# Kernel optimization log

Hardware: AMD Instinct MI355X
Metric: run time of the kernel (lower is better)

Reference implementation:

```python
import jax, jax.numpy as jnp
import numpy as np

# SqueezeSeg CRF config
NUM_CLASS = 4
SIZE_Z, SIZE_A = 3, 5            # LCN_HEIGHT, LCN_WIDTH
B, H, W = 16, 64, 512            # batch, zenith, azimuth
RCRF_ITER = 3
BI_FILTER_COEF = 0.1
ANG_FILTER_COEF = 0.02
ANG_THETA_A = 0.9
BILATERAL_THETA_A = 0.9
K = SIZE_Z * SIZE_A              # 15 -> 14 neighbors (center excluded)

# neighbor offsets of the 3x5 condensing kernel, center excluded
OFFSETS = [(dz, da) for dz in range(SIZE_Z) for da in range(SIZE_A)
           if not (dz == SIZE_Z // 2 and da == SIZE_A // 2)]

def _gauss_weights(theta_sq):
    # angular_filter_kernel: Gaussian of squared spatial offset, center zeroed
    g = [np.exp(-((dz - SIZE_Z // 2) ** 2 + (da - SIZE_A // 2) ** 2) / (2.0 * theta_sq))
         for dz, da in OFFSETS]
    return jnp.asarray(np.array(g, dtype=np.float32))

def gather_neighbors(x):
    # x: [B,C,H,W] -> [B,C,K-1,H,W]; zero-padded 'same' neighborhood gather
    pz, pa = SIZE_Z // 2, SIZE_A // 2
    xp = jnp.pad(x, ((0, 0), (0, 0), (pz, pz), (pa, pa)))
    return jnp.stack([xp[:, :, dz:dz + H, da:da + W] for dz, da in OFFSETS], axis=2)

def setup_inputs() -> dict:
    key = jax.random.key(0)
    k1, k2, k3 = jax.random.split(key, 3)
    x = jax.random.normal(k1, (B, NUM_CLASS, H, W), dtype=jnp.float32)
    bilateral_filters = jax.random.uniform(k2, (B, 1, K - 1, H, W), dtype=jnp.float32)
    lidar_mask = (jax.random.uniform(k3, (B, 1, H, W)) > 0.5).astype(jnp.float32)
    return {"x": x, "bilateral_filters": bilateral_filters, "lidar_mask": lidar_mask}

def reference(x, bilateral_filters, lidar_mask):
    g_ang = _gauss_weights(ANG_THETA_A ** 2)
    g_bi = _gauss_weights(BILATERAL_THETA_A ** 2)
    compat = jnp.ones((NUM_CLASS, NUM_CLASS), jnp.float32) - jnp.eye(NUM_CLASS, dtype=jnp.float32)
    ang_compat = compat * ANG_FILTER_COEF   # [out_class, in_class] 1x1 conv
    bi_compat = compat * BI_FILTER_COEF

    for _ in range(RCRF_ITER):
        unary = jax.nn.softmax(x, axis=1)                     # softmax over class dim
        nb = gather_neighbors(unary)                          # [B,C,14,H,W]
        # depthwise angular filters = Gaussian-weighted neighbor sums
        ang = jnp.einsum('k,bckhw->bchw', g_ang, nb)
        bi_ang = jnp.einsum('k,bckhw->bchw', g_bi, nb)
        # condensing conv on masked unary, weighted by per-pixel bilateral filters
        nb_m = gather_neighbors(unary * lidar_mask)           # [B,C,14,H,W]
        condensed = jnp.sum(nb_m * bilateral_filters, axis=2) # [B,C,H,W]
        bi = condensed * lidar_mask * bi_ang
        # 1x1 compatibility transforms
        ang2 = jnp.einsum('oc,bchw->bohw', ang_compat, ang)
        bi2 = jnp.einsum('oc,bchw->bohw', bi_compat, bi)
        x = unary + ang2 + bi2
    return x
```

## Files before the change

### kernel.cpp

```cpp
#include <hip/hip_runtime.h>


#define NCLASS 4
#define HH 64
#define WW 512
#define BB 16
#define TH 8
#define TW 64
#define UR (TH + 6)
#define UC (TW + 12)
#define PLANE (HH * WW)

#define G1 0.53940412f
#define G2 0.29095687f
#define G4 0.08466190f
#define G5 0.04566227f

__device__ __forceinline__ void fma4(float4& d, float s, const float4& v) {
    d.x = fmaf(s, v.x, d.x);
    d.y = fmaf(s, v.y, d.y);
    d.z = fmaf(s, v.z, d.z);
    d.w = fmaf(s, v.w, d.w);
}

template <bool SM>
__device__ __forceinline__ float4 crf_combine(const float4 A, const float4 C,
                                              const float4 u, const float mcen)
{
    const float bx = C.x * mcen * A.x;
    const float by = C.y * mcen * A.y;
    const float bz = C.z * mcen * A.z;
    const float bw = C.w * mcen * A.w;
    const float sa = A.x + A.y + A.z + A.w;
    const float sb = bx + by + bz + bw;
    float4 r;
    r.x = u.x + 0.02f * (sa - A.x) + 0.1f * (sb - bx);
    r.y = u.y + 0.02f * (sa - A.y) + 0.1f * (sb - by);
    r.z = u.z + 0.02f * (sa - A.z) + 0.1f * (sb - bz);
    r.w = u.w + 0.02f * (sa - A.w) + 0.1f * (sb - bw);
    if (SM) {
        const float mx  = fmaxf(fmaxf(r.x, r.y), fmaxf(r.z, r.w));
        const float e0  = __expf(r.x - mx);
        const float e1  = __expf(r.y - mx);
        const float e2  = __expf(r.z - mx);
        const float e3  = __expf(r.w - mx);
        const float inv = 1.0f / (e0 + e1 + e2 + e3);
        r = make_float4(e0 * inv, e1 * inv, e2 * inv, e3 * inv);
    }
    return r;
}

template <int MR, int MC, bool FINAL>
__device__ __forceinline__ void crf_step(
    float4 (*__restrict__ u_lds)[UC], const float (*__restrict__ m_lds)[UC],
    const float* __restrict__ filt, float* __restrict__ dst,
    int b, int h0, int w0, int tid)
{
    constexpr int RH  = TH + 2 * MR;
    constexpr int RW  = TW + 2 * MC;
    constexpr int GPR = RW / 2;
    constexpr int NG  = RH * GPR;
    constexpr int NS  = (NG + 255) / 256;

    const float GE[5] = {G5, G2, G1, G2, G5};
    const float GC[5] = {G4, G1, 0.f, G1, G4};

    float4 xa[NS], xb[NS];

#pragma unroll
    for (int j = 0; j < NS; ++j) {
        const int s = tid + 256 * j;
        float4 r0 = make_float4(0.f, 0.f, 0.f, 0.f);
        float4 r1 = make_float4(0.f, 0.f, 0.f, 0.f);
        int gh = -1, gw = -1;
        if (s < NG) {
            const int lr = s / GPR;
            const int gc = s - lr * GPR;
            const int lc = 2 * gc;
            gh = h0 + lr - MR;
            gw = w0 + lc - MC;
            const int ur = lr + (3 - MR);
            const int uc = lc + (6 - MC);
            if (gh >= 0 && gh < HH && gw >= 0 && gw < WW) {
                const float* fp = filt + ((size_t)b * 14 * HH + gh) * WW + gw;
                float2 f[14];
#pragma unroll
                for (int k = 0; k < 14; ++k)
                    f[k] = *reinterpret_cast<const float2*>(fp + (size_t)k * PLANE);

                float4 A0 = make_float4(0.f, 0.f, 0.f, 0.f);
                float4 A1 = A0, C0 = A0, C1 = A0;
                float4 ucen0 = A0, ucen1 = A0;
                float  mcen0 = 0.f, mcen1 = 0.f;

#pragma unroll
                for (int dz = -1; dz <= 1; ++dz) {
                    const int rr = ur + dz;
                    float4 U[6];
                    float  M[6];
#pragma unroll
                    for (int t = 0; t < 6; ++t) U[t] = u_lds[rr][uc - 2 + t];
#pragma unroll
                    for (int t = 0; t < 3; ++t) {
                        const float2 mm =
                            *reinterpret_cast<const float2*>(&m_lds[rr][uc - 2 + 2 * t]);
                        M[2 * t]     = mm.x;
                        M[2 * t + 1] = mm.y;
                    }
                    if (dz == 0) { ucen0 = U[2]; ucen1 = U[3]; mcen0 = M[2]; mcen1 = M[3]; }
#pragma unroll
                    for (int t = 0; t < 5; ++t) {
                        if (dz == 0 && t == 2) continue;
                        const int   k  = (dz == -1) ? t
                                       : (dz == 0)  ? 5 + (t > 2 ? t - 1 : t)
                                                    : 9 + t;
                        const float gk = (dz == 0) ? GC[t] : GE[t];
                        const float fm0 = f[k].x * M[t];
                        const float fm1 = f[k].y * M[t + 1];
                        fma4(A0, gk,  U[t]);      fma4(C0, fm0, U[t]);
                        fma4(A1, gk,  U[t + 1]);  fma4(C1, fm1, U[t + 1]);
                    }
                }
                r0 = crf_combine<!FINAL>(A0, C0, ucen0, mcen0);
                r1 = crf_combine<!FINAL>(A1, C1, ucen1, mcen1);

                if (FINAL) {
                    float* o = dst + ((size_t)b * NCLASS * HH + gh) * WW + gw;
                    *reinterpret_cast<float2*>(o)             = make_float2(r0.x, r1.x);
                    *reinterpret_cast<float2*>(o + PLANE)     = make_float2(r0.y, r1.y);
                    *reinterpret_cast<float2*>(o + 2 * PLANE) = make_float2(r0.z, r1.z);
                    *reinterpret_cast<float2*>(o + 3 * PLANE) = make_float2(r0.w, r1.w);
                }
            }
        }
        if (!FINAL) { xa[j] = r0; xb[j] = r1; }
    }

    if (!FINAL) {
        __syncthreads();
#pragma unroll
        for (int j = 0; j < NS; ++j) {
            const int s = tid + 256 * j;
            if (s < NG) {
                const int lr = s / GPR;
                const int gc = s - lr * GPR;
                const int lc = 2 * gc;
                u_lds[lr + (3 - MR)][lc + (6 - MC)]     = xa[j];
                u_lds[lr + (3 - MR)][lc + (6 - MC) + 1] = xb[j];
            }
        }
        __syncthreads();
    }
}

__global__ __launch_bounds__(256, 4) void crf_fused(
    const float* __restrict__ xin,
    const float* __restrict__ filt,
    const float* __restrict__ mask,
    float* __restrict__ xout)
{
    __shared__ float4 u_lds[UR][UC];
    __shared__ float  m_lds[UR][UC];

    const int b   = blockIdx.z;
    const int h0  = blockIdx.y * TH;
    const int w0  = blockIdx.x * TW;
    const int tid = threadIdx.x;

    constexpr int NP = (UR * UC) / 2;
    for (int idx = tid; idx < NP; idx += 256) {
        const int lr = idx / (UC / 2);
        const int lc = 2 * (idx - lr * (UC / 2));
        const int gh = h0 + lr - 3;
        const int gw = w0 + lc - 6;
        float4 u0 = make_float4(0.f, 0.f, 0.f, 0.f);
        float4 u1 = u0;
        float2 mm = make_float2(0.f, 0.f);
        if (gh >= 0 && gh < HH && gw >= 0 && gw < WW) {
            const float* px = xin + ((size_t)b * NCLASS * HH + gh) * WW + gw;
            const float2 v0 = *reinterpret_cast<const float2*>(px);
            const float2 v1 = *reinterpret_cast<const float2*>(px + PLANE);
            const float2 v2 = *reinterpret_cast<const float2*>(px + 2 * PLANE);
            const float2 v3 = *reinterpret_cast<const float2*>(px + 3 * PLANE);
            mm = *reinterpret_cast<const float2*>(mask + ((size_t)b * HH + gh) * WW + gw);
            {
                const float mx  = fmaxf(fmaxf(v0.x, v1.x), fmaxf(v2.x, v3.x));
                const float e0  = __expf(v0.x - mx);
                const float e1  = __expf(v1.x - mx);
                const float e2  = __expf(v2.x - mx);
                const float e3  = __expf(v3.x - mx);
                const float inv = 1.0f / (e0 + e1 + e2 + e3);
                u0 = make_float4(e0 * inv, e1 * inv, e2 * inv, e3 * inv);
            }
            {
                const float mx  = fmaxf(fmaxf(v0.y, v1.y), fmaxf(v2.y, v3.y));
                const float e0  = __expf(v0.y - mx);
                const float e1  = __expf(v1.y - mx);
                const float e2  = __expf(v2.y - mx);
                const float e3  = __expf(v3.y - mx);
                const float inv = 1.0f / (e0 + e1 + e2 + e3);
                u1 = make_float4(e0 * inv, e1 * inv, e2 * inv, e3 * inv);
            }
        }
        u_lds[lr][lc]     = u0;
        u_lds[lr][lc + 1] = u1;
        *reinterpret_cast<float2*>(&m_lds[lr][lc]) = mm;
    }
    __syncthreads();

    crf_step<2, 4, false>(u_lds, m_lds, filt, xout, b, h0, w0, tid);
    crf_step<1, 2, false>(u_lds, m_lds, filt, xout, b, h0, w0, tid);
    crf_step<0, 0, true >(u_lds, m_lds, filt, xout, b, h0, w0, tid);
}

extern "C" void kernel_launch(void* const* d_in, const int* in_sizes, int n_in,
                              void* d_out, int out_size, void* d_ws, size_t ws_size,
                              hipStream_t stream) {
    const float* x    = (const float*)d_in[0];
    const float* filt = (const float*)d_in[1];
    const float* msk  = (const float*)d_in[2];
    float* out = (float*)d_out;
    (void)d_ws; (void)ws_size;

    dim3 grid(WW / TW, HH / TH, BB);
    dim3 block(256);
    crf_fused<<<grid, block, 0, stream>>>(x, filt, msk, out);
}
```

Before: 100.0 us.

## Map one thread per pixel pair and load bilateral filters once for all CRF iterations

Switches to 512-thread blocks with a fixed pixel-pair assignment per thread covering the largest halo region (12x72). Each thread loads its 14 bilateral filter values into registers once and reuses them across all three CRF iterations, instead of reloading them from global memory every iteration. Later iterations, which cover smaller regions, leave some threads idle, and holding the filters in registers raises register pressure at 512 threads per block.

Measured after the change: 96.14 us. -3.9%, faster.

```diff
diff --git a/kernel.cpp b/kernel.cpp
--- a/kernel.cpp
+++ b/kernel.cpp
@@ -10,6 +10,10 @@
 #define UR (TH + 6)
 #define UC (TW + 12)
 #define PLANE (HH * WW)
+#define R1H 12
+#define R1W 72
+#define GPR1 (R1W / 2)
+#define NPAIR1 (R1H * GPR1)
 
 #define G1 0.53940412f
 #define G2 0.29095687f
@@ -53,107 +57,83 @@
 template <int MR, int MC, bool FINAL>
 __device__ __forceinline__ void crf_step(
     float4 (*__restrict__ u_lds)[UC], const float (*__restrict__ m_lds)[UC],
-    const float* __restrict__ filt, float* __restrict__ dst,
-    int b, int h0, int w0, int tid)
+    const float2* __restrict__ f, float* __restrict__ dst,
+    int b, int lr1, int lc1, int gh, int gw, bool inb)
 {
-    constexpr int RH  = TH + 2 * MR;
-    constexpr int RW  = TW + 2 * MC;
-    constexpr int GPR = RW / 2;
-    constexpr int NG  = RH * GPR;
-    constexpr int NS  = (NG + 255) / 256;
+    constexpr int RH = TH + 2 * MR;
+    constexpr int RW = TW + 2 * MC;
+    constexpr int LR_LO = 2 - MR, LR_HI = 2 - MR + RH;
+    constexpr int LC_LO = 4 - MC, LC_HI = 4 - MC + RW;
+
+    const bool act = inb && lr1 >= LR_LO && lr1 < LR_HI
+                         && lc1 >= LC_LO && (lc1 + 1) < LC_HI;
 
     const float GE[5] = {G5, G2, G1, G2, G5};
     const float GC[5] = {G4, G1, 0.f, G1, G4};
 
-    float4 xa[NS], xb[NS];
-
-#pragma unroll
-    for (int j = 0; j < NS; ++j) {
-        const int s = tid + 256 * j;
-        float4 r0 = make_float4(0.f, 0.f, 0.f, 0.f);
-        float4 r1 = make_float4(0.f, 0.f, 0.f, 0.f);
-        int gh = -1, gw = -1;
-        if (s < NG) {
-            const int lr = s / GPR;
-            const int gc = s - lr * GPR;
-            const int lc = 2 * gc;
-            gh = h0 + lr - MR;
-            gw = w0 + lc - MC;
-            const int ur = lr + (3 - MR);
-            const int uc = lc + (6 - MC);
-            if (gh >= 0 && gh < HH && gw >= 0 && gw < WW) {
-                const float* fp = filt + ((size_t)b * 14 * HH + gh) * WW + gw;
-                float2 f[14];
-#pragma unroll
-                for (int k = 0; k < 14; ++k)
-                    f[k] = *reinterpret_cast<const float2*>(fp + (size_t)k * PLANE);
-
-                float4 A0 = make_float4(0.f, 0.f, 0.f, 0.f);
-                float4 A1 = A0, C0 = A0, C1 = A0;
-                float4 ucen0 = A0, ucen1 = A0;
-                float  mcen0 = 0.f, mcen1 = 0.f;
-
-#pragma unroll
-                for (int dz = -1; dz <= 1; ++dz) {
-                    const int rr = ur + dz;
-                    float4 U[6];
-                    float  M[6];
-#pragma unroll
-                    for (int t = 0; t < 6; ++t) U[t] = u_lds[rr][uc - 2 + t];
-#pragma unroll
-                    for (int t = 0; t < 3; ++t) {
-                        const float2 mm =
-                            *reinterpret_cast<const float2*>(&m_lds[rr][uc - 2 + 2 * t]);
-                        M[2 * t]     = mm.x;
-                        M[2 * t + 1] = mm.y;
-                    }
-                    if (dz == 0) { ucen0 = U[2]; ucen1 = U[3]; mcen0 = M[2]; mcen1 = M[3]; }
-#pragma unroll
-                    for (int t = 0; t < 5; ++t) {
-                        if (dz == 0 && t == 2) continue;
-                        const int   k  = (dz == -1) ? t
-                                       : (dz == 0)  ? 5 + (t > 2 ? t - 1 : t)
-                                                    : 9 + t;
-                        const float gk = (dz == 0) ? GC[t] : GE[t];
-                        const float fm0 = f[k].x * M[t];
-                        const float fm1 = f[k].y * M[t + 1];
-                        fma4(A0, gk,  U[t]);      fma4(C0, fm0, U[t]);
-                        fma4(A1, gk,  U[t + 1]);  fma4(C1, fm1, U[t + 1]);
-                    }
-                }
-                r0 = crf_combine<!FINAL>(A0, C0, ucen0, mcen0);
-                r1 = crf_combine<!FINAL>(A1, C1, ucen1, mcen1);
-
-                if (FINAL) {
-                    float* o = dst + ((size_t)b * NCLASS * HH + gh) * WW + gw;
-                    *reinterpret_cast<float2*>(o)             = make_float2(r0.x, r1.x);
-                    *reinterpret_cast<float2*>(o + PLANE)     = make_float2(r0.y, r1.y);
-                    *reinterpret_cast<float2*>(o + 2 * PLANE) = make_float2(r0.z, r1.z);
-                    *reinterpret_cast<float2*>(o + 3 * PLANE) = make_float2(r0.w, r1.w);
-                }
-            }
-        }
-        if (!FINAL) { xa[j] = r0; xb[j] = r1; }
+    float4 r0 = make_float4(0.f, 0.f, 0.f, 0.f);
+    float4 r1 = r0;
+
+    if (act) {
+        const int ur = lr1 + 1;
+        const int uc = lc1 + 2;
+
+        float4 A0 = make_float4(0.f, 0.f, 0.f, 0.f);
+        float4 A1 = A0, C0 = A0, C1 = A0;
+        float4 ucen0 = A0, ucen1 = A0;
+        float  mcen0 = 0.f, mcen1 = 0.f;
+
+#pragma unroll
+        for (int dz = -1; dz <= 1; ++dz) {
+            const int rr = ur + dz;
+            float4 U[6];
+            float  M[6];
+#pragma unroll
+            for (int t = 0; t < 6; ++t) U[t] = u_lds[rr][uc - 2 + t];
+#pragma unroll
+            for (int t = 0; t < 3; ++t) {
+                const float2 mm =
+                    *reinterpret_cast<const float2*>(&m_lds[rr][uc - 2 + 2 * t]);
+                M[2 * t]     = mm.x;
+                M[2 * t + 1] = mm.y;
+            }
+            if (dz == 0) { ucen0 = U[2]; ucen1 = U[3]; mcen0 = M[2]; mcen1 = M[3]; }
+#pragma unroll
+            for (int t = 0; t < 5; ++t) {
+                if (dz == 0 && t == 2) continue;
+                const int   k  = (dz == -1) ? t
+                               : (dz == 0)  ? 5 + (t > 2 ? t - 1 : t)
+                                            : 9 + t;
+                const float gk = (dz == 0) ? GC[t] : GE[t];
+                const float fm0 = f[k].x * M[t];
+                const float fm1 = f[k].y * M[t + 1];
+                fma4(A0, gk,  U[t]);      fma4(C0, fm0, U[t]);
+                fma4(A1, gk,  U[t + 1]);  fma4(C1, fm1, U[t + 1]);
+            }
+        }
+        r0 = crf_combine<!FINAL>(A0, C0, ucen0, mcen0);
+        r1 = crf_combine<!FINAL>(A1, C1, ucen1, mcen1);
+
+        if (FINAL) {
+            float* o = dst + ((size_t)b * NCLASS * HH + gh) * WW + gw;
+            *reinterpret_cast<float2*>(o)             = make_float2(r0.x, r1.x);
+            *reinterpret_cast<float2*>(o + PLANE)     = make_float2(r0.y, r1.y);
+            *reinterpret_cast<float2*>(o + 2 * PLANE) = make_float2(r0.z, r1.z);
+            *reinterpret_cast<float2*>(o + 3 * PLANE) = make_float2(r0.w, r1.w);
+        }
     }
 
     if (!FINAL) {
         __syncthreads();
-#pragma unroll
-        for (int j = 0; j < NS; ++j) {
-            const int s = tid + 256 * j;
-            if (s < NG) {
-                const int lr = s / GPR;
-                const int gc = s - lr * GPR;
-                const int lc = 2 * gc;
-                u_lds[lr + (3 - MR)][lc + (6 - MC)]     = xa[j];
-                u_lds[lr + (3 - MR)][lc + (6 - MC) + 1] = xb[j];
-            }
+        if (act) {
+            u_lds[lr1 + 1][lc1 + 2] = r0;
+            u_lds[lr1 + 1][lc1 + 3] = r1;
         }
         __syncthreads();
     }
 }
 
-__global__ __launch_bounds__(256, 4) void crf_fused(
+__global__ __launch_bounds__(512, 4) void crf_fused(
     const float* __restrict__ xin,
     const float* __restrict__ filt,
     const float* __restrict__ mask,
@@ -168,21 +148,21 @@
     const int tid = threadIdx.x;
 
     constexpr int NP = (UR * UC) / 2;
-    for (int idx = tid; idx < NP; idx += 256) {
+    for (int idx = tid; idx < NP; idx += 512) {
         const int lr = idx / (UC / 2);
         const int lc = 2 * (idx - lr * (UC / 2));
-        const int gh = h0 + lr - 3;
-        const int gw = w0 + lc - 6;
+        const int ph = h0 + lr - 3;
+        const int pw = w0 + lc - 6;
         float4 u0 = make_float4(0.f, 0.f, 0.f, 0.f);
         float4 u1 = u0;
         float2 mm = make_float2(0.f, 0.f);
-        if (gh >= 0 && gh < HH && gw >= 0 && gw < WW) {
-            const float* px = xin + ((size_t)b * NCLASS * HH + gh) * WW + gw;
+        if (ph >= 0 && ph < HH && pw >= 0 && pw < WW) {
+            const float* px = xin + ((size_t)b * NCLASS * HH + ph) * WW + pw;
             const float2 v0 = *reinterpret_cast<const float2*>(px);
             const float2 v1 = *reinterpret_cast<const float2*>(px + PLANE);
             const float2 v2 = *reinterpret_cast<const float2*>(px + 2 * PLANE);
             const float2 v3 = *reinterpret_cast<const float2*>(px + 3 * PLANE);
-            mm = *reinterpret_cast<const float2*>(mask + ((size_t)b * HH + gh) * WW + gw);
+            mm = *reinterpret_cast<const float2*>(mask + ((size_t)b * HH + ph) * WW + pw);
             {
                 const float mx  = fmaxf(fmaxf(v0.x, v1.x), fmaxf(v2.x, v3.x));
                 const float e0  = __expf(v0.x - mx);
@@ -208,9 +188,24 @@
     }
     __syncthreads();
 
-    crf_step<2, 4, false>(u_lds, m_lds, filt, xout, b, h0, w0, tid);
-    crf_step<1, 2, false>(u_lds, m_lds, filt, xout, b, h0, w0, tid);
-    crf_step<0, 0, true >(u_lds, m_lds, filt, xout, b, h0, w0, tid);
+    const int  p   = tid;
+    const int  lr1 = p / GPR1;
+    const int  lc1 = 2 * (p - lr1 * GPR1);
+    const int  gh  = h0 + lr1 - 2;
+    const int  gw  = w0 + lc1 - 4;
+    const bool inb = (p < NPAIR1) && gh >= 0 && gh < HH && gw >= 0 && gw < WW;
+
+    float2 f[14];
+    if (inb) {
+        const float* fp = filt + ((size_t)b * 14 * HH + gh) * WW + gw;
+#pragma unroll
+        for (int k = 0; k < 14; ++k)
+            f[k] = *reinterpret_cast<const float2*>(fp + (size_t)k * PLANE);
+    }
+
+    crf_step<2, 4, false>(u_lds, m_lds, f, xout, b, lr1, lc1, gh, gw, inb);
+    crf_step<1, 2, false>(u_lds, m_lds, f, xout, b, lr1, lc1, gh, gw, inb);
+    crf_step<0, 0, true >(u_lds, m_lds, f, xout, b, lr1, lc1, gh, gw, inb);
 }
 
 extern "C" void kernel_launch(void* const* d_in, const int* in_sizes, int n_in,
@@ -223,6 +218,6 @@
     (void)d_ws; (void)ws_size;
 
     dim3 grid(WW / TW, HH / TH, BB);
-    dim3 block(256);
+    dim3 block(512);
     crf_fused<<<grid, block, 0, stream>>>(x, filt, msk, out);
 }
```
